# Kernel tuning notes

Hardware: AMD Instinct MI355X
Metric: run time of the kernel (lower is better)

## Reference

```python
import jax, jax.numpy as jnp
import numpy as np

P, N, NF = 4, 871, 512            # num_meta_paths, node_size (hardcoded 871 in source), node_feature_size
XDIM = 116 * 116                   # x_proj input dim, hardcoded Linear(116*116, nf)
BETA, LAMBDA_WL, GAMMA = 0.1, 0.1, 0.1


def _xavier(k, shape):
    fan_in, fan_out = shape[0], shape[-1]
    bound = np.sqrt(6.0 / (fan_in + fan_out))
    return jax.random.uniform(k, shape, jnp.float32, -bound, bound)


def setup_inputs() -> dict:
    key = jax.random.key(0)
    ks = jax.random.split(key, 12)
    return {
        "z_stack": jax.random.normal(ks[0], (P, N, NF), jnp.float32),
        "x_orig": jax.random.normal(ks[1], (1, 116, 116), jnp.float32),
        "W": _xavier(ks[2], (N, 1)),
        "b": jax.random.uniform(ks[3], (N, 1), jnp.float32),
        "q": _xavier(ks[4], (N, NF)),
        "xp_w": _xavier(ks[5], (XDIM, NF)),
        "xp_b": jnp.zeros((NF,), jnp.float32),
        "w1": _xavier(ks[6], (2 * NF, 512)), "b1": jnp.zeros((512,), jnp.float32),
        "w2": _xavier(ks[7], (512, 256)), "b2": jnp.zeros((256,), jnp.float32),
        "w3": _xavier(ks[8], (256, 1)), "b3": jnp.zeros((1,), jnp.float32),
        "perm": jax.random.permutation(ks[9], N).astype(jnp.int32),
    }


def _mi_mlp(t, w1, b1, w2, b2, w3, b3):
    h = jax.nn.relu(t @ w1 + b1)
    h = jax.nn.relu(h @ w2 + b2)
    return h @ w3 + b3  # [N, 1]


def reference(z_stack, x_orig, W, b, q, xp_w, xp_b, w1, b1, w2, b2, w3, b3, perm):
    # --- vectorized form of the per-node loop:
    # score_p = mean_i( tanh(W_i * z[p,i,:] + b_i) . q_i )
    zt = jnp.tanh(W[None] * z_stack + b[None])            # [P,N,NF]
    scores = jnp.mean(jnp.sum(zt * q[None], axis=-1), axis=-1)  # [P]
    proportions = scores / jnp.sum(scores)
    attn = jax.nn.softmax(proportions)                    # [P] (no isomorphic pairs -> no overwrite)
    # layer_out_p = attn_p * z_p + z_p ; emb = sum_p layer_out_p
    emb = jnp.einsum('p,pnf->nf', 1.0 + attn, z_stack)    # [N,NF]
    # --- estimate_MI(x_orig, emb, mi_estimator_xz)
    x = jnp.broadcast_to(x_orig.reshape(1, -1), (N, XDIM))
    xh = x @ xp_w + xp_b                                  # [N,NF]
    t0 = jnp.concatenate([xh, emb], axis=1)               # [N,2NF]
    t1 = jnp.concatenate([xh, emb[perm]], axis=1)
    mi_lb = jnp.mean(_mi_mlp(t0, w1, b1, w2, b2, w3, b3)) - jnp.log(
        jnp.mean(jnp.exp(_mi_mlp(t1, w1, b1, w2, b2, w3, b3))) + 1e-8)
    I_XZ = jnp.clip(mi_lb, 0.0)
    # y_labels=None -> I_ZY = 0 ; empty isomorphic_pairs -> wl_loss = 0
    total_loss = I_XZ - BETA * 0.0 + LAMBDA_WL * 0.0 + GAMMA * jnp.sum(attn)
    return emb, total_loss
```

## Files before the change

kernel.cpp:

```cpp
#include <hip/hip_runtime.h>
#include <hip/hip_bf16.h>
#include <math.h>

#define NMETA  4
#define NNODE  871
#define NFEAT  512
#define XDIM   (116*116)
#define ZPLANE (NNODE*NFEAT)
#define NCHUNK 55
#define MT     55

#define WS_COEF   8
#define WS_CNT    12
#define WS_SPART  16
#define WS_C1P    256
#define WS_XHP    8448
#define WS_V      73984
#define WS_W1P    74856
#define WS_W2P    205928

typedef short v8s __attribute__((ext_vector_type(8)));
typedef float v4f __attribute__((ext_vector_type(4)));

static __device__ __forceinline__ short f2bf(float f) {
  __hip_bfloat16 h = __float2bfloat16(f);
  return *reinterpret_cast<short*>(&h);
}

__global__ __launch_bounds__(256) void k_front(const float* __restrict__ x,
                                               const float* __restrict__ xpw,
                                               const float* __restrict__ w1,
                                               const float* __restrict__ w2,
                                               const float* __restrict__ z,
                                               const float* __restrict__ W,
                                               const float* __restrict__ b,
                                               const float* __restrict__ q,
                                               float* __restrict__ ws,
                                               short* __restrict__ w1p,
                                               short* __restrict__ w2p) {
  const int blk = blockIdx.x;
  const int tid = threadIdx.x;
  if (blk < 128) {
    const int f4 = tid & 127;
    const int rp = tid >> 7;
    const int d0 = blk * 106;
    const int rows = min(106, XDIM - d0);
    __shared__ float xs[106];
    if (tid < rows) xs[tid] = x[d0 + tid];
    __syncthreads();
    float4 acc = {0.f, 0.f, 0.f, 0.f};
    const float4* xp4 = (const float4*)xpw;
#pragma unroll 4
    for (int r = rp; r < rows; r += 2) {
      const float xv = xs[r];
      const float4 w = xp4[(size_t)(d0 + r) * 128 + f4];
      acc.x += xv * w.x; acc.y += xv * w.y; acc.z += xv * w.z; acc.w += xv * w.w;
    }
    __shared__ float4 red4[128];
    if (rp) red4[f4] = acc;
    __syncthreads();
    if (!rp) {
      float4 o = red4[f4];
      o.x += acc.x; o.y += acc.y; o.z += acc.z; o.w += acc.w;
      ((float4*)(ws + WS_XHP + (size_t)blk * NFEAT))[f4] = o;
    }
  } else if (blk < 512) {
    const int base = (blk - 128) * 256 + tid;
#pragma unroll
    for (int it = 0; it < 4; ++it) {
      int t = base + it * 98304;
      if (t < 262144) {
        int j = t & 7; int r = t >> 3;
        int n15 = r & 15; r >>= 4;
        int quad = r & 3; r >>= 2;
        int nt = r & 31; int kb = r >> 5;
        int k = kb * 32 + quad * 8 + j;
        int n = nt * 16 + n15;
        w1p[t] = f2bf(w1[(size_t)(512 + k) * 512 + n]);
      } else {
        int o = t - 262144;
        int j = o & 7; int r = o >> 3;
        int n15 = r & 15; r >>= 4;
        int quad = r & 3; r >>= 2;
        int nt = r & 15; int kb = r >> 4;
        int k = kb * 32 + quad * 8 + j;
        int n = nt * 16 + n15;
        w2p[o] = f2bf(w2[(size_t)k * 256 + n]);
      }
    }
  } else {
    const int sblk = blk - 512;
    const int p = sblk / NCHUNK;
    const int chunk = sblk % NCHUNK;
    const int i0 = chunk * 16;
    const int i1 = min(i0 + 16, NNODE);
    const int f4 = tid & 127;
    const int ip = tid >> 7;
    float local = 0.f;
    for (int i = i0 + ip; i < i1; i += 2) {
      const float wi = W[i];
      const float bi = b[i];
      const float4 zr = ((const float4*)(z + ((size_t)p * NNODE + i) * NFEAT))[f4];
      const float4 qr = ((const float4*)(q + (size_t)i * NFEAT))[f4];
      local += tanhf(wi * zr.x + bi) * qr.x + tanhf(wi * zr.y + bi) * qr.y
             + tanhf(wi * zr.z + bi) * qr.z + tanhf(wi * zr.w + bi) * qr.w;
    }
    __shared__ float red[256];
    red[tid] = local;
    __syncthreads();
    for (int s = 128; s > 0; s >>= 1) {
      if (tid < s) red[tid] += red[tid + s];
      __syncthreads();
    }
    if (tid == 0) ws[WS_SPART + sblk] = red[0];
  }
}

__global__ __launch_bounds__(256) void k_prep(const float* __restrict__ xpb,
                                              const float* __restrict__ w1,
                                              const float* __restrict__ b1,
                                              float* __restrict__ ws) {
  const int tid = threadIdx.x;
  if (blockIdx.x < 16) {
    const int bk = blockIdx.x;
    __shared__ float xs[32];
    {
      const int f = tid & 31;
      const int pg = tid >> 5;
      float s = 0.f;
#pragma unroll 4
      for (int p = pg; p < 128; p += 8)
        s += ws[WS_XHP + (size_t)p * NFEAT + bk * 32 + f];
      __shared__ float red[256];
      red[tid] = s;
      __syncthreads();
      if (tid < 32) {
        float t2 = 0.f;
#pragma unroll
        for (int g = 0; g < 8; ++g) t2 += red[g * 32 + tid];
        xs[tid] = t2 + xpb[bk * 32 + tid];
      }
      __syncthreads();
    }
    const int j4 = tid & 127;
    const int fp = tid >> 7;
    float4 acc = {0.f, 0.f, 0.f, 0.f};
    const float4* w14 = (const float4*)w1;
#pragma unroll
    for (int ff = 0; ff < 16; ++ff) {
      const int f = bk * 32 + fp * 16 + ff;
      const float xv = xs[fp * 16 + ff];
      const float4 w = w14[(size_t)f * 128 + j4];
      acc.x += xv * w.x; acc.y += xv * w.y; acc.z += xv * w.z; acc.w += xv * w.w;
    }
    __shared__ float4 red2[128];
    if (fp) red2[j4] = acc;
    __syncthreads();
    if (!fp) {
      float4 o = red2[j4];
      o.x += acc.x; o.y += acc.y; o.z += acc.z; o.w += acc.w;
      if (bk == 0) {
        o.x += b1[j4 * 4 + 0]; o.y += b1[j4 * 4 + 1];
        o.z += b1[j4 * 4 + 2]; o.w += b1[j4 * 4 + 3];
      }
      ((float4*)(ws + WS_C1P + (size_t)bk * NFEAT))[j4] = o;
    }
  } else {
    __shared__ float sp[220];
    if (tid < 220) sp[tid] = ws[WS_SPART + tid];
    __syncthreads();
    if (tid == 0) {
      float sv[NMETA], sum = 0.f;
#pragma unroll
      for (int p = 0; p < NMETA; ++p) {
        float s = 0.f;
        for (int c = 0; c < NCHUNK; ++c) s += sp[p * NCHUNK + c];
        sv[p] = s / (float)NNODE;
        sum += sv[p];
      }
      float m = -1e30f;
#pragma unroll
      for (int p = 0; p < NMETA; ++p) { sv[p] = sv[p] / sum; m = fmaxf(m, sv[p]); }
      float es = 0.f;
#pragma unroll
      for (int p = 0; p < NMETA; ++p) { sv[p] = expf(sv[p] - m); es += sv[p]; }
#pragma unroll
      for (int p = 0; p < NMETA; ++p) ws[WS_COEF + p] = 1.f + sv[p] / es;
      *(unsigned int*)&ws[WS_CNT] = 0u;
    }
    for (int i = tid; i < NNODE; i += 256) ws[WS_V + i] = 0.f;
  }
}

__global__ __launch_bounds__(256) void k_fused(const float* __restrict__ z,
                                               float* __restrict__ ws,
                                               float* __restrict__ out,
                                               const short* __restrict__ w1p,
                                               const short* __restrict__ w2p,
                                               const float* __restrict__ b2,
                                               const float* __restrict__ w3,
                                               const float* __restrict__ b3) {
  __shared__ __align__(16) short embs[8192];
  __shared__ __align__(16) short h2a[8192];
  __shared__ float cs[512];
  __shared__ float rf0[256], rf1[256];
  const int tid = threadIdx.x;
  const int r0 = blockIdx.x * 16;

  {
    float a0 = 0.f, a1 = 0.f;
#pragma unroll
    for (int k = 0; k < 16; ++k) {
      a0 += ws[WS_C1P + k * 512 + tid];
      a1 += ws[WS_C1P + k * 512 + 256 + tid];
    }
    cs[tid] = a0;
    cs[256 + tid] = a1;
  }
  const float c0 = ws[WS_COEF + 0], c1c = ws[WS_COEF + 1];
  const float c2 = ws[WS_COEF + 2], c3 = ws[WS_COEF + 3];

  const int oc = tid & 63;
  const float4* z4 = (const float4*)z;
  float4* out4 = (float4*)out;
#pragma unroll
  for (int t = 0; t < 4; ++t) {
    const int row = (tid >> 6) + 4 * t;
    const int gr = r0 + row;
    const int slot = oc * 16 + (row ^ (oc & 15));
    v8s h;
    if (gr < NNODE) {
      const int zi = gr * 128 + oc * 2;
      float4 a0 = z4[zi],               a1 = z4[zi + 1];
      float4 b0 = z4[NNODE*128 + zi],   b1 = z4[NNODE*128 + zi + 1];
      float4 d0 = z4[2*NNODE*128 + zi], d1 = z4[2*NNODE*128 + zi + 1];
      float4 e0 = z4[3*NNODE*128 + zi], e1 = z4[3*NNODE*128 + zi + 1];
      float4 r0v, r1v;
      r0v.x = c0*a0.x + c1c*b0.x + c2*d0.x + c3*e0.x;
      r0v.y = c0*a0.y + c1c*b0.y + c2*d0.y + c3*e0.y;
      r0v.z = c0*a0.z + c1c*b0.z + c2*d0.z + c3*e0.z;
      r0v.w = c0*a0.w + c1c*b0.w + c2*d0.w + c3*e0.w;
      r1v.x = c0*a1.x + c1c*b1.x + c2*d1.x + c3*e1.x;
      r1v.y = c0*a1.y + c1c*b1.y + c2*d1.y + c3*e1.y;
      r1v.z = c0*a1.z + c1c*b1.z + c2*d1.z + c3*e1.z;
      r1v.w = c0*a1.w + c1c*b1.w + c2*d1.w + c3*e1.w;
      out4[zi] = r0v;
      out4[zi + 1] = r1v;
      h[0] = f2bf(r0v.x); h[1] = f2bf(r0v.y); h[2] = f2bf(r0v.z); h[3] = f2bf(r0v.w);
      h[4] = f2bf(r1v.x); h[5] = f2bf(r1v.y); h[6] = f2bf(r1v.z); h[7] = f2bf(r1v.w);
    } else {
      h = (v8s){0,0,0,0,0,0,0,0};
    }
    *(v8s*)(embs + slot * 8) = h;
  }
  __syncthreads();

  const int lane = tid & 63, w = tid >> 6;
  const int n15 = lane & 15, quad = lane >> 4;
  v4f e[8];
#pragma unroll
  for (int ct = 0; ct < 8; ++ct) e[ct] = (v4f){0.f, 0.f, 0.f, 0.f};
#pragma unroll
  for (int kb = 0; kb < 16; ++kb) {
    const int koct = kb * 4 + quad;
    v8s a = *(const v8s*)(embs + (koct * 16 + (n15 ^ (koct & 15))) * 8);
    const short* B = w1p + kb * 16384 + w * 4096 + quad * 128 + n15 * 8;
#pragma unroll
    for (int ct = 0; ct < 8; ++ct) {
      v8s bb = *(const v8s*)(B + ct * 512);
      e[ct] = __builtin_amdgcn_mfma_f32_16x16x32_bf16(a, bb, e[ct], 0, 0, 0);
    }
  }
#pragma unroll
  for (int ct = 0; ct < 8; ++ct) {
    const int col = w * 128 + ct * 16 + n15;
    const int koct = col >> 3, j = col & 7;
#pragma unroll
    for (int r = 0; r < 4; ++r) {
      const int m = quad * 4 + r;
      h2a[(koct * 16 + (m ^ (koct & 15))) * 8 + j] = f2bf(fmaxf(e[ct][r] + cs[col], 0.f));
    }
  }
  __syncthreads();

  v4f g[4];
#pragma unroll
  for (int ct = 0; ct < 4; ++ct) g[ct] = (v4f){0.f, 0.f, 0.f, 0.f};
#pragma unroll
  for (int kb = 0; kb < 16; ++kb) {
    const int koct = kb * 4 + quad;
    v8s a = *(const v8s*)(h2a + (koct * 16 + (n15 ^ (koct & 15))) * 8);
    const short* B = w2p + kb * 8192 + w * 2048 + quad * 128 + n15 * 8;
#pragma unroll
    for (int ct = 0; ct < 4; ++ct) {
      v8s bb = *(const v8s*)(B + ct * 512);
      g[ct] = __builtin_amdgcn_mfma_f32_16x16x32_bf16(a, bb, g[ct], 0, 0, 0);
    }
  }
#pragma unroll
  for (int r = 0; r < 4; ++r) {
    float s = 0.f;
#pragma unroll
    for (int ct = 0; ct < 4; ++ct) {
      const int col = w * 64 + ct * 16 + n15;
      s += fmaxf(g[ct][r] + b2[col], 0.f) * w3[col];
    }
    s += __shfl_xor(s, 1);
    s += __shfl_xor(s, 2);
    s += __shfl_xor(s, 4);
    s += __shfl_xor(s, 8);
    const int grow = r0 + quad * 4 + r;
    if (n15 == 0 && grow < NNODE) atomicAdd(&ws[WS_V + grow], s);
  }

  __shared__ unsigned last;
  __syncthreads();
  if (tid == 0) {
    __threadfence();
    unsigned old = atomicAdd((unsigned int*)&ws[WS_CNT], 1u);
    last = (old == MT - 1) ? 1u : 0u;
  }
  __syncthreads();
  if (last) {
    const float bias = b3[0];
    float s0 = 0.f, s1 = 0.f;
    for (int i = tid; i < NNODE; i += 256) {
      float xv = __hip_atomic_load(&ws[WS_V + i], __ATOMIC_RELAXED, __HIP_MEMORY_SCOPE_AGENT) + bias;
      s0 += xv;
      s1 += expf(xv);
    }
    rf0[tid] = s0; rf1[tid] = s1;
    __syncthreads();
    for (int s = 128; s > 0; s >>= 1) {
      if (tid < s) { rf0[tid] += rf0[tid + s]; rf1[tid] += rf1[tid + s]; }
      __syncthreads();
    }
    if (tid == 0) {
      float m0 = rf0[0] / (float)NNODE;
      float m1 = rf1[0] / (float)NNODE;
      float mi = m0 - logf(m1 + 1e-8f);
      out[ZPLANE] = fmaxf(mi, 0.f) + 0.1f;
    }
  }
}

extern "C" void kernel_launch(void* const* d_in, const int* in_sizes, int n_in,
                              void* d_out, int out_size, void* d_ws, size_t ws_size,
                              hipStream_t stream) {
  const float* z   = (const float*)d_in[0];
  const float* x   = (const float*)d_in[1];
  const float* W   = (const float*)d_in[2];
  const float* b   = (const float*)d_in[3];
  const float* q   = (const float*)d_in[4];
  const float* xpw = (const float*)d_in[5];
  const float* xpb = (const float*)d_in[6];
  const float* w1  = (const float*)d_in[7];
  const float* b1  = (const float*)d_in[8];
  const float* w2  = (const float*)d_in[9];
  const float* b2  = (const float*)d_in[10];
  const float* w3  = (const float*)d_in[11];
  const float* b3  = (const float*)d_in[12];
  float* out = (float*)d_out;
  float* ws  = (float*)d_ws;

  short* w1p = (short*)(ws + WS_W1P);
  short* w2p = (short*)(ws + WS_W2P);

  k_front<<<732, 256, 0, stream>>>(x, xpw, w1, w2, z, W, b, q, ws, w1p, w2p);
  k_prep<<<17, 256, 0, stream>>>(xpb, w1, b1, ws);
  k_fused<<<MT, 256, 0, stream>>>(z, ws, out, w1p, w2p, b2, w3, b3);
}
```

Measured before the change: 133.2 us.

## Split fused MLP kernel: move emb build to prep, split GEMM1 across N halves

The emb combine and bf16 packing move out of the 55-block fused kernel into a 220-block prep kernel, which writes packed tiles to workspace. The first MLP GEMM is split into two column halves across 110 blocks, and the second block to finish each row tile runs GEMM2, chosen through a per-tile atomic flag. The x_proj reduction is spread over 256 blocks instead of 128. This raises parallelism on a GPU with many compute units. The cost is extra global round trips for emb and h2a and another level of atomic handoff.

```diff
diff --git a/kernel.cpp b/kernel.cpp
--- a/kernel.cpp
+++ b/kernel.cpp
@@ -10,14 +10,16 @@
 #define NCHUNK 55
 #define MT     55
 
-#define WS_COEF   8
-#define WS_CNT    12
 #define WS_SPART  16
 #define WS_C1P    256
 #define WS_XHP    8448
-#define WS_V      73984
-#define WS_W1P    74856
-#define WS_W2P    205928
+#define WS_V      139520
+#define WS_CNT    140392
+#define WS_FLAGS  140400
+#define WS_EMBBP  140464
+#define WS_H2AP   369840
+#define WS_W1P    599216
+#define WS_W2P    730288
 
 typedef short v8s __attribute__((ext_vector_type(8)));
 typedef float v4f __attribute__((ext_vector_type(4)));
@@ -40,12 +42,12 @@
                                                short* __restrict__ w2p) {
   const int blk = blockIdx.x;
   const int tid = threadIdx.x;
-  if (blk < 128) {
+  if (blk < 256) {
     const int f4 = tid & 127;
     const int rp = tid >> 7;
-    const int d0 = blk * 106;
-    const int rows = min(106, XDIM - d0);
-    __shared__ float xs[106];
+    const int d0 = blk * 53;
+    const int rows = min(53, XDIM - d0);
+    __shared__ float xs[53];
     if (tid < rows) xs[tid] = x[d0 + tid];
     __syncthreads();
     float4 acc = {0.f, 0.f, 0.f, 0.f};
@@ -64,8 +66,8 @@
       o.x += acc.x; o.y += acc.y; o.z += acc.z; o.w += acc.w;
       ((float4*)(ws + WS_XHP + (size_t)blk * NFEAT))[f4] = o;
     }
-  } else if (blk < 512) {
-    const int base = (blk - 128) * 256 + tid;
+  } else if (blk < 640) {
+    const int base = (blk - 256) * 256 + tid;
 #pragma unroll
     for (int it = 0; it < 4; ++it) {
       int t = base + it * 98304;
@@ -89,7 +91,7 @@
       }
     }
   } else {
-    const int sblk = blk - 512;
+    const int sblk = blk - 640;
     const int p = sblk / NCHUNK;
     const int chunk = sblk % NCHUNK;
     const int i0 = chunk * 16;
@@ -116,123 +118,45 @@
   }
 }
 
-__global__ __launch_bounds__(256) void k_prep(const float* __restrict__ xpb,
-                                              const float* __restrict__ w1,
-                                              const float* __restrict__ b1,
-                                              float* __restrict__ ws) {
+__global__ __launch_bounds__(256) void k_prep2(const float* __restrict__ z,
+                                               const float* __restrict__ xpb,
+                                               const float* __restrict__ w1,
+                                               const float* __restrict__ b1,
+                                               float* __restrict__ ws,
+                                               float* __restrict__ out,
+                                               short* __restrict__ embp) {
   const int tid = threadIdx.x;
-  if (blockIdx.x < 16) {
-    const int bk = blockIdx.x;
-    __shared__ float xs[32];
-    {
-      const int f = tid & 31;
-      const int pg = tid >> 5;
-      float s = 0.f;
-#pragma unroll 4
-      for (int p = pg; p < 128; p += 8)
-        s += ws[WS_XHP + (size_t)p * NFEAT + bk * 32 + f];
-      __shared__ float red[256];
-      red[tid] = s;
-      __syncthreads();
-      if (tid < 32) {
-        float t2 = 0.f;
-#pragma unroll
-        for (int g = 0; g < 8; ++g) t2 += red[g * 32 + tid];
-        xs[tid] = t2 + xpb[bk * 32 + tid];
-      }
-      __syncthreads();
-    }
-    const int j4 = tid & 127;
-    const int fp = tid >> 7;
-    float4 acc = {0.f, 0.f, 0.f, 0.f};
-    const float4* w14 = (const float4*)w1;
-#pragma unroll
-    for (int ff = 0; ff < 16; ++ff) {
-      const int f = bk * 32 + fp * 16 + ff;
-      const float xv = xs[fp * 16 + ff];
-      const float4 w = w14[(size_t)f * 128 + j4];
-      acc.x += xv * w.x; acc.y += xv * w.y; acc.z += xv * w.z; acc.w += xv * w.w;
-    }
-    __shared__ float4 red2[128];
-    if (fp) red2[j4] = acc;
-    __syncthreads();
-    if (!fp) {
-      float4 o = red2[j4];
-      o.x += acc.x; o.y += acc.y; o.z += acc.z; o.w += acc.w;
-      if (bk == 0) {
-        o.x += b1[j4 * 4 + 0]; o.y += b1[j4 * 4 + 1];
-        o.z += b1[j4 * 4 + 2]; o.w += b1[j4 * 4 + 3];
-      }
-      ((float4*)(ws + WS_C1P + (size_t)bk * NFEAT))[j4] = o;
-    }
-  } else {
+  if (blockIdx.x < 220) {
     __shared__ float sp[220];
     if (tid < 220) sp[tid] = ws[WS_SPART + tid];
     __syncthreads();
-    if (tid == 0) {
-      float sv[NMETA], sum = 0.f;
-#pragma unroll
-      for (int p = 0; p < NMETA; ++p) {
-        float s = 0.f;
-        for (int c = 0; c < NCHUNK; ++c) s += sp[p * NCHUNK + c];
-        sv[p] = s / (float)NNODE;
-        sum += sv[p];
-      }
-      float m = -1e30f;
-#pragma unroll
-      for (int p = 0; p < NMETA; ++p) { sv[p] = sv[p] / sum; m = fmaxf(m, sv[p]); }
-      float es = 0.f;
-#pragma unroll
-      for (int p = 0; p < NMETA; ++p) { sv[p] = expf(sv[p] - m); es += sv[p]; }
-#pragma unroll
-      for (int p = 0; p < NMETA; ++p) ws[WS_COEF + p] = 1.f + sv[p] / es;
-      *(unsigned int*)&ws[WS_CNT] = 0u;
-    }
-    for (int i = tid; i < NNODE; i += 256) ws[WS_V + i] = 0.f;
-  }
-}
-
-__global__ __launch_bounds__(256) void k_fused(const float* __restrict__ z,
-                                               float* __restrict__ ws,
-                                               float* __restrict__ out,
-                                               const short* __restrict__ w1p,
-                                               const short* __restrict__ w2p,
-                                               const float* __restrict__ b2,
-                                               const float* __restrict__ w3,
-                                               const float* __restrict__ b3) {
-  __shared__ __align__(16) short embs[8192];
-  __shared__ __align__(16) short h2a[8192];
-  __shared__ float cs[512];
-  __shared__ float rf0[256], rf1[256];
-  const int tid = threadIdx.x;
-  const int r0 = blockIdx.x * 16;
-
-  {
-    float a0 = 0.f, a1 = 0.f;
-#pragma unroll
-    for (int k = 0; k < 16; ++k) {
-      a0 += ws[WS_C1P + k * 512 + tid];
-      a1 += ws[WS_C1P + k * 512 + 256 + tid];
-    }
-    cs[tid] = a0;
-    cs[256 + tid] = a1;
-  }
-  const float c0 = ws[WS_COEF + 0], c1c = ws[WS_COEF + 1];
-  const float c2 = ws[WS_COEF + 2], c3 = ws[WS_COEF + 3];
-
-  const int oc = tid & 63;
-  const float4* z4 = (const float4*)z;
-  float4* out4 = (float4*)out;
-#pragma unroll
-  for (int t = 0; t < 4; ++t) {
-    const int row = (tid >> 6) + 4 * t;
-    const int gr = r0 + row;
-    const int slot = oc * 16 + (row ^ (oc & 15));
+    float sv[NMETA], sum = 0.f;
+#pragma unroll
+    for (int p = 0; p < NMETA; ++p) {
+      float s = 0.f;
+      for (int c = 0; c < NCHUNK; ++c) s += sp[p * NCHUNK + c];
+      sv[p] = s / (float)NNODE;
+      sum += sv[p];
+    }
+    float m = -1e30f;
+#pragma unroll
+    for (int p = 0; p < NMETA; ++p) { sv[p] = sv[p] / sum; m = fmaxf(m, sv[p]); }
+    float es = 0.f;
+#pragma unroll
+    for (int p = 0; p < NMETA; ++p) { sv[p] = expf(sv[p] - m); es += sv[p]; }
+    const float c0 = 1.f + sv[0] / es, c1c = 1.f + sv[1] / es;
+    const float c2 = 1.f + sv[2] / es, c3 = 1.f + sv[3] / es;
+
+    const int mt = blockIdx.x >> 2;
+    const int rl = (blockIdx.x & 3) * 4 + (tid >> 6);
+    const int gr = mt * 16 + rl;
+    const int oc = tid & 63;
     v8s h;
     if (gr < NNODE) {
+      const float4* z4 = (const float4*)z;
       const int zi = gr * 128 + oc * 2;
       float4 a0 = z4[zi],               a1 = z4[zi + 1];
-      float4 b0 = z4[NNODE*128 + zi],   b1 = z4[NNODE*128 + zi + 1];
+      float4 b0 = z4[NNODE*128 + zi],   b1v = z4[NNODE*128 + zi + 1];
       float4 d0 = z4[2*NNODE*128 + zi], d1 = z4[2*NNODE*128 + zi + 1];
       float4 e0 = z4[3*NNODE*128 + zi], e1 = z4[3*NNODE*128 + zi + 1];
       float4 r0v, r1v;
@@ -240,106 +164,189 @@
       r0v.y = c0*a0.y + c1c*b0.y + c2*d0.y + c3*e0.y;
       r0v.z = c0*a0.z + c1c*b0.z + c2*d0.z + c3*e0.z;
       r0v.w = c0*a0.w + c1c*b0.w + c2*d0.w + c3*e0.w;
-      r1v.x = c0*a1.x + c1c*b1.x + c2*d1.x + c3*e1.x;
-      r1v.y = c0*a1.y + c1c*b1.y + c2*d1.y + c3*e1.y;
-      r1v.z = c0*a1.z + c1c*b1.z + c2*d1.z + c3*e1.z;
-      r1v.w = c0*a1.w + c1c*b1.w + c2*d1.w + c3*e1.w;
-      out4[zi] = r0v;
-      out4[zi + 1] = r1v;
+      r1v.x = c0*a1.x + c1c*b1v.x + c2*d1.x + c3*e1.x;
+      r1v.y = c0*a1.y + c1c*b1v.y + c2*d1.y + c3*e1.y;
+      r1v.z = c0*a1.z + c1c*b1v.z + c2*d1.z + c3*e1.z;
+      r1v.w = c0*a1.w + c1c*b1v.w + c2*d1.w + c3*e1.w;
+      ((float4*)out)[zi] = r0v;
+      ((float4*)out)[zi + 1] = r1v;
       h[0] = f2bf(r0v.x); h[1] = f2bf(r0v.y); h[2] = f2bf(r0v.z); h[3] = f2bf(r0v.w);
       h[4] = f2bf(r1v.x); h[5] = f2bf(r1v.y); h[6] = f2bf(r1v.z); h[7] = f2bf(r1v.w);
     } else {
       h = (v8s){0,0,0,0,0,0,0,0};
     }
-    *(v8s*)(embs + slot * 8) = h;
-  }
-  __syncthreads();
-
+    *(v8s*)(embp + ((size_t)(mt * 64 + oc) * 16 + rl) * 8) = h;
+  } else if (blockIdx.x < 236) {
+    const int bk = blockIdx.x - 220;
+    __shared__ float xs[32];
+    {
+      const int f = tid & 31;
+      const int pg = tid >> 5;
+      float s = 0.f;
+#pragma unroll 4
+      for (int p = pg; p < 256; p += 8)
+        s += ws[WS_XHP + (size_t)p * NFEAT + bk * 32 + f];
+      __shared__ float red[256];
+      red[tid] = s;
+      __syncthreads();
+      if (tid < 32) {
+        float t2 = 0.f;
+#pragma unroll
+        for (int g = 0; g < 8; ++g) t2 += red[g * 32 + tid];
+        xs[tid] = t2 + xpb[bk * 32 + tid];
+      }
+      __syncthreads();
+    }
+    const int j4 = tid & 127;
+    const int fp = tid >> 7;
+    float4 acc = {0.f, 0.f, 0.f, 0.f};
+    const float4* w14 = (const float4*)w1;
+#pragma unroll
+    for (int ff = 0; ff < 16; ++ff) {
+      const int f = bk * 32 + fp * 16 + ff;
+      const float xv = xs[fp * 16 + ff];
+      const float4 w = w14[(size_t)f * 128 + j4];
+      acc.x += xv * w.x; acc.y += xv * w.y; acc.z += xv * w.z; acc.w += xv * w.w;
+    }
+    __shared__ float4 red2[128];
+    if (fp) red2[j4] = acc;
+    __syncthreads();
+    if (!fp) {
+      float4 o = red2[j4];
+      o.x += acc.x; o.y += acc.y; o.z += acc.z; o.w += acc.w;
+      if (bk == 0) {
+        o.x += b1[j4 * 4 + 0]; o.y += b1[j4 * 4 + 1];
+        o.z += b1[j4 * 4 + 2]; o.w += b1[j4 * 4 + 3];
+      }
+      ((float4*)(ws + WS_C1P + (size_t)bk * NFEAT))[j4] = o;
+    }
+  } else {
+    for (int i = tid; i < NNODE; i += 256) ws[WS_V + i] = 0.f;
+    if (tid == 0) *(unsigned int*)&ws[WS_CNT] = 0u;
+    if (tid < MT) ((unsigned int*)&ws[WS_FLAGS])[tid] = 0u;
+  }
+}
+
+__global__ __launch_bounds__(256) void k_gemmAll(float* __restrict__ ws,
+                                                 float* __restrict__ out,
+                                                 const short* __restrict__ embp,
+                                                 short* __restrict__ h2ap,
+                                                 const short* __restrict__ w1p,
+                                                 const short* __restrict__ w2p,
+                                                 const float* __restrict__ b2,
+                                                 const float* __restrict__ w3,
+                                                 const float* __restrict__ b3) {
+  const int tid = threadIdx.x;
+  const int mt = blockIdx.x >> 1;
+  const int nh = blockIdx.x & 1;
   const int lane = tid & 63, w = tid >> 6;
   const int n15 = lane & 15, quad = lane >> 4;
-  v4f e[8];
-#pragma unroll
-  for (int ct = 0; ct < 8; ++ct) e[ct] = (v4f){0.f, 0.f, 0.f, 0.f};
+
+  __shared__ float cs[256];
+  {
+    float a = 0.f;
+#pragma unroll
+    for (int k = 0; k < 16; ++k) a += ws[WS_C1P + k * 512 + nh * 256 + tid];
+    cs[tid] = a;
+  }
+  __syncthreads();
+
+  v4f e[4];
+#pragma unroll
+  for (int ct = 0; ct < 4; ++ct) e[ct] = (v4f){0.f, 0.f, 0.f, 0.f};
 #pragma unroll
   for (int kb = 0; kb < 16; ++kb) {
     const int koct = kb * 4 + quad;
-    v8s a = *(const v8s*)(embs + (koct * 16 + (n15 ^ (koct & 15))) * 8);
-    const short* B = w1p + kb * 16384 + w * 4096 + quad * 128 + n15 * 8;
-#pragma unroll
-    for (int ct = 0; ct < 8; ++ct) {
+    v8s a = *(const v8s*)(embp + ((size_t)(mt * 64 + koct) * 16 + n15) * 8);
+    const short* B = w1p + kb * 16384 + (nh * 16 + w * 4) * 512 + quad * 128 + n15 * 8;
+#pragma unroll
+    for (int ct = 0; ct < 4; ++ct) {
       v8s bb = *(const v8s*)(B + ct * 512);
       e[ct] = __builtin_amdgcn_mfma_f32_16x16x32_bf16(a, bb, e[ct], 0, 0, 0);
     }
   }
 #pragma unroll
-  for (int ct = 0; ct < 8; ++ct) {
-    const int col = w * 128 + ct * 16 + n15;
+  for (int ct = 0; ct < 4; ++ct) {
+    const int cl = w * 64 + ct * 16 + n15;
+    const int col = nh * 256 + cl;
     const int koct = col >> 3, j = col & 7;
 #pragma unroll
     for (int r = 0; r < 4; ++r) {
       const int m = quad * 4 + r;
-      h2a[(koct * 16 + (m ^ (koct & 15))) * 8 + j] = f2bf(fmaxf(e[ct][r] + cs[col], 0.f));
-    }
-  }
-  __syncthreads();
-
-  v4f g[4];
-#pragma unroll
-  for (int ct = 0; ct < 4; ++ct) g[ct] = (v4f){0.f, 0.f, 0.f, 0.f};
-#pragma unroll
-  for (int kb = 0; kb < 16; ++kb) {
-    const int koct = kb * 4 + quad;
-    v8s a = *(const v8s*)(h2a + (koct * 16 + (n15 ^ (koct & 15))) * 8);
-    const short* B = w2p + kb * 8192 + w * 2048 + quad * 128 + n15 * 8;
-#pragma unroll
-    for (int ct = 0; ct < 4; ++ct) {
-      v8s bb = *(const v8s*)(B + ct * 512);
-      g[ct] = __builtin_amdgcn_mfma_f32_16x16x32_bf16(a, bb, g[ct], 0, 0, 0);
-    }
-  }
-#pragma unroll
-  for (int r = 0; r < 4; ++r) {
-    float s = 0.f;
-#pragma unroll
-    for (int ct = 0; ct < 4; ++ct) {
-      const int col = w * 64 + ct * 16 + n15;
-      s += fmaxf(g[ct][r] + b2[col], 0.f) * w3[col];
-    }
-    s += __shfl_xor(s, 1);
-    s += __shfl_xor(s, 2);
-    s += __shfl_xor(s, 4);
-    s += __shfl_xor(s, 8);
-    const int grow = r0 + quad * 4 + r;
-    if (n15 == 0 && grow < NNODE) atomicAdd(&ws[WS_V + grow], s);
-  }
-
-  __shared__ unsigned last;
+      h2ap[((size_t)(mt * 64 + koct) * 16 + m) * 8 + j] = f2bf(fmaxf(e[ct][r] + cs[cl], 0.f));
+    }
+  }
+
+  __shared__ int win;
   __syncthreads();
   if (tid == 0) {
     __threadfence();
-    unsigned old = atomicAdd((unsigned int*)&ws[WS_CNT], 1u);
-    last = (old == MT - 1) ? 1u : 0u;
+    unsigned old = atomicAdd((unsigned int*)&ws[WS_FLAGS] + mt, 1u);
+    win = (old == 1u) ? 1 : 0;
   }
   __syncthreads();
-  if (last) {
-    const float bias = b3[0];
-    float s0 = 0.f, s1 = 0.f;
-    for (int i = tid; i < NNODE; i += 256) {
-      float xv = __hip_atomic_load(&ws[WS_V + i], __ATOMIC_RELAXED, __HIP_MEMORY_SCOPE_AGENT) + bias;
-      s0 += xv;
-      s1 += expf(xv);
-    }
-    rf0[tid] = s0; rf1[tid] = s1;
-    __syncthreads();
-    for (int s = 128; s > 0; s >>= 1) {
-      if (tid < s) { rf0[tid] += rf0[tid + s]; rf1[tid] += rf1[tid + s]; }
+  if (win) {
+    __threadfence();
+    v4f g[4];
+#pragma unroll
+    for (int ct = 0; ct < 4; ++ct) g[ct] = (v4f){0.f, 0.f, 0.f, 0.f};
+#pragma unroll
+    for (int kb = 0; kb < 16; ++kb) {
+      const int koct = kb * 4 + quad;
+      v8s a = *(const v8s*)(h2ap + ((size_t)(mt * 64 + koct) * 16 + n15) * 8);
+      const short* B = w2p + kb * 8192 + (w * 4) * 512 + quad * 128 + n15 * 8;
+#pragma unroll
+      for (int ct = 0; ct < 4; ++ct) {
+        v8s bb = *(const v8s*)(B + ct * 512);
+        g[ct] = __builtin_amdgcn_mfma_f32_16x16x32_bf16(a, bb, g[ct], 0, 0, 0);
+      }
+    }
+#pragma unroll
+    for (int r = 0; r < 4; ++r) {
+      float s = 0.f;
+#pragma unroll
+      for (int ct = 0; ct < 4; ++ct) {
+        const int col = w * 64 + ct * 16 + n15;
+        s += fmaxf(g[ct][r] + b2[col], 0.f) * w3[col];
+      }
+      s += __shfl_xor(s, 1);
+      s += __shfl_xor(s, 2);
+      s += __shfl_xor(s, 4);
+      s += __shfl_xor(s, 8);
+      const int grow = mt * 16 + quad * 4 + r;
+      if (n15 == 0 && grow < NNODE) atomicAdd(&ws[WS_V + grow], s);
+    }
+
+    __shared__ int last;
+    __syncthreads();
+    if (tid == 0) {
+      __threadfence();
+      unsigned old = atomicAdd((unsigned int*)&ws[WS_CNT], 1u);
+      last = (old == MT - 1) ? 1 : 0;
+    }
+    __syncthreads();
+    if (last) {
+      __shared__ float rf0[256], rf1[256];
+      const float bias = b3[0];
+      float s0 = 0.f, s1 = 0.f;
+      for (int i = tid; i < NNODE; i += 256) {
+        float xv = __hip_atomic_load(&ws[WS_V + i], __ATOMIC_RELAXED,
+                                     __HIP_MEMORY_SCOPE_AGENT) + bias;
+        s0 += xv;
+        s1 += expf(xv);
+      }
+      rf0[tid] = s0; rf1[tid] = s1;
       __syncthreads();
-    }
-    if (tid == 0) {
-      float m0 = rf0[0] / (float)NNODE;
-      float m1 = rf1[0] / (float)NNODE;
-      float mi = m0 - logf(m1 + 1e-8f);
-      out[ZPLANE] = fmaxf(mi, 0.f) + 0.1f;
+      for (int s = 128; s > 0; s >>= 1) {
+        if (tid < s) { rf0[tid] += rf0[tid + s]; rf1[tid] += rf1[tid + s]; }
+        __syncthreads();
+      }
+      if (tid == 0) {
+        float m0 = rf0[0] / (float)NNODE;
+        float m1 = rf1[0] / (float)NNODE;
+        float mi = m0 - logf(m1 + 1e-8f);
+        out[ZPLANE] = fmaxf(mi, 0.f) + 0.1f;
+      }
     }
   }
 }
@@ -363,10 +370,12 @@
   float* out = (float*)d_out;
   float* ws  = (float*)d_ws;
 
-  short* w1p = (short*)(ws + WS_W1P);
-  short* w2p = (short*)(ws + WS_W2P);
-
-  k_front<<<732, 256, 0, stream>>>(x, xpw, w1, w2, z, W, b, q, ws, w1p, w2p);
-  k_prep<<<17, 256, 0, stream>>>(xpb, w1, b1, ws);
-  k_fused<<<MT, 256, 0, stream>>>(z, ws, out, w1p, w2p, b2, w3, b3);
-}
+  short* embp = (short*)(ws + WS_EMBBP);
+  short* h2ap = (short*)(ws + WS_H2AP);
+  short* w1p  = (short*)(ws + WS_W1P);
+  short* w2p  = (short*)(ws + WS_W2P);
+
+  k_front<<<860, 256, 0, stream>>>(x, xpw, w1, w2, z, W, b, q, ws, w1p, w2p);
+  k_prep2<<<237, 256, 0, stream>>>(z, xpb, w1, b1, ws, out, embp);
+  k_gemmAll<<<110, 256, 0, stream>>>(ws, out, embp, h2ap, w1p, w2p, b2, w3, b3);
+}
```

After: 141.7 us. 1.06x slower.
